# Performance work log

Measured on AMD Instinct MI355X. Metric: run time of the kernel, lower is better.

## Reference

```python
import jax, jax.numpy as jnp
import numpy as np

H = 512        # rnn_h
E = 256        # embedding_dim
ATD = 32       # action_type_emb_dim
VOCAB = 50000  # data_agent.wordcnt
NUM_ACTIONS = 10
CHECK_WEIGHT = 1.0
B, SIN, SOUT, Y = 32, 128, 32, 256
DIN = 2 * H + 1 + E + ATD + E  # dec_gru input size (y_in=True, bidir=True)


def gru_step(h, x, Wih, Whh, bih, bhh):
    # PyTorch GRUCell math
    gi = x @ Wih.T + bih
    gh = h @ Whh.T + bhh
    ir, iz, i_n = jnp.split(gi, 3, axis=-1)
    hr, hz, h_n = jnp.split(gh, 3, axis=-1)
    r = jax.nn.sigmoid(ir + hr)
    z = jax.nn.sigmoid(iz + hz)
    n = jnp.tanh(i_n + r * h_n)
    return (1.0 - z) * n + z * h


def setup_inputs() -> dict:
    key = jax.random.key(0)
    ks = iter(jax.random.split(key, 48))

    def p(shape, scale=0.05):
        return jax.random.normal(next(ks), shape, dtype=jnp.float32) * scale

    inp = {}
    inp["x"] = jax.random.randint(next(ks), (B, SIN), 0, VOCAB)
    inp["action_key"] = jax.random.randint(next(ks), (Y,), 0, VOCAB)
    inp["action_type"] = jax.random.randint(next(ks), (Y,), 0, NUM_ACTIONS + 1)
    inp["current_room"] = jax.random.randint(next(ks), (B, SOUT), 0, VOCAB)
    inp["checked"] = jax.random.uniform(next(ks), (B, SOUT + 1, Y), dtype=jnp.float32)
    inp["y"] = jax.random.uniform(next(ks), (B, SOUT, Y), dtype=jnp.float32)
    emb = p((VOCAB, E))
    inp["emb_table"] = emb.at[0].set(0.0)  # padding_idx=0
    inp["atype_table"] = p((NUM_ACTIONS + 1, ATD))
    # encoder GRU, bidirectional, 1 layer
    inp["enc_Wih_f"] = p((3 * H, E)); inp["enc_Whh_f"] = p((3 * H, H))
    inp["enc_bih_f"] = p((3 * H,));   inp["enc_bhh_f"] = p((3 * H,))
    inp["enc_Wih_b"] = p((3 * H, E)); inp["enc_Whh_b"] = p((3 * H, H))
    inp["enc_bih_b"] = p((3 * H,));   inp["enc_bhh_b"] = p((3 * H,))
    inp["trans_W"] = p((E, 2 * H)); inp["trans_b"] = p((E,))
    inp["merge_W"] = p((H, 2 * H)); inp["merge_b"] = p((H,))
    inp["dec_Wih"] = p((3 * H, DIN)); inp["dec_Whh"] = p((3 * H, H))
    inp["dec_bih"] = p((3 * H,));     inp["dec_bhh"] = p((3 * H,))
    inp["dec_W"] = p((1, H)); inp["dec_b"] = p((1,))
    inp["chk_W1"] = p((H, 2 * H + ATD + H)); inp["chk_b1"] = p((H,))
    inp["chk_W2"] = p((1, H));               inp["chk_b2"] = p((1,))
    return inp


def reference(x, action_key, action_type, current_room, checked, y,
              emb_table, atype_table,
              enc_Wih_f, enc_Whh_f, enc_bih_f, enc_bhh_f,
              enc_Wih_b, enc_Whh_b, enc_bih_b, enc_bhh_b,
              trans_W, trans_b, merge_W, merge_b,
              dec_Wih, dec_Whh, dec_bih, dec_bhh, dec_W, dec_b,
              chk_W1, chk_b1, chk_W2, chk_b2):
    emb_out = emb_table[x]  # [B, SIN, E]

    def enc_scan(Wih, Whh, bih, bhh, xs):  # xs: [S, B, E]
        def step(h, xt):
            h2 = gru_step(h, xt, Wih, Whh, bih, bhh)
            return h2, h2
        h0 = jnp.zeros((B, H), emb_out.dtype)
        return jax.lax.scan(step, h0, xs)

    xs = emb_out.transpose(1, 0, 2)
    hT_f, hs_f = enc_scan(enc_Wih_f, enc_Whh_f, enc_bih_f, enc_bhh_f, xs)
    hT_b, hs_b = enc_scan(enc_Wih_b, enc_Whh_b, enc_bih_b, enc_bhh_b, xs[::-1])
    hs_b = hs_b[::-1]
    enc_out = jnp.concatenate([hs_f, hs_b], axis=-1).transpose(1, 0, 2)  # [B, SIN, 2H]

    action_emb = emb_table[action_key]  # [Y, E]
    trans_out = jnp.tanh(enc_out @ trans_W.T + trans_b)  # [B, SIN, E]
    scores = (jnp.einsum('bse,ye->bys', emb_out, action_emb)
              + jnp.einsum('bse,ye->bys', trans_out, action_emb))
    alpha = jax.nn.softmax(scores, axis=-1)
    attention = jnp.einsum('bys,bsd->byd', alpha, enc_out)  # [B, Y, 2H]

    atype_exp = jnp.broadcast_to(atype_table[action_type], (B, Y, ATD))
    room_emb = emb_table[current_room]  # [B, SOUT, E]

    # faithful to torch: hidden [2,B,H].view(B, 2H) (layer-major flatten)
    hidden_cat = jnp.stack([hT_f, hT_b], 0).reshape(B, 2 * H)
    h0_dec = jnp.tanh(hidden_cat @ merge_W.T + merge_b)  # [B, H]
    h_dec = jnp.broadcast_to(h0_dec[:, None, :], (B, Y, H)).reshape(B * Y, H)

    y_prev = jnp.concatenate([jnp.zeros((B, 1, Y), y.dtype), y[:, :-1]], axis=1)

    att_flat = attention.reshape(B * Y, 2 * H)
    at_flat = atype_exp.reshape(B * Y, ATD)

    xs_scan = (checked[:, :SOUT].transpose(1, 0, 2),   # check_in  [T,B,Y]
               room_emb.transpose(1, 0, 2),            # room      [T,B,E]
               y_prev.transpose(1, 0, 2),              # y_{t-1}   [T,B,Y]
               y.transpose(1, 0, 2),                   # y_t       [T,B,Y]
               checked[:, 1:].transpose(1, 0, 2))      # check tgt [T,B,Y]

    def step(h, inputs):
        chk_t, room_t, yp_t, y_t, chk_next = inputs
        room_in = jnp.broadcast_to(room_t[:, None, :], (B, Y, E))
        y_in = jnp.broadcast_to((yp_t @ action_emb)[:, None, :], (B, Y, E))
        dec_in = jnp.concatenate(
            [attention, chk_t[..., None], room_in, atype_exp, y_in], axis=-1
        ).reshape(B * Y, DIN)
        h2 = gru_step(h, dec_in, dec_Wih, dec_Whh, dec_bih, dec_bhh)
        logits = (h2 @ dec_W.T + dec_b).reshape(B, Y)
        logp = jax.nn.log_softmax(logits, axis=1)
        l = -(logp * y_t).sum()
        cat = jnp.concatenate([att_flat, at_flat, h2], axis=1)
        chk = jax.nn.sigmoid(jnp.tanh(cat @ chk_W1.T + chk_b1) @ chk_W2.T + chk_b2).reshape(B, Y)
        cl = -((chk_next * jnp.log(chk) + (1.0 - chk_next) * jnp.log(1.0 - chk)) * y_t).sum() * CHECK_WEIGHT
        return h2, (l, cl)

    _, (ls, cls) = jax.lax.scan(step, h_dec, xs_scan)
    ysum = y.sum()
    loss = ls.sum() / ysum
    check_loss = cls.sum() / ysum
    return (loss + check_loss, loss, check_loss)
```

## Files before the change

kernel.cpp:

```cpp
#include <hip/hip_runtime.h>

typedef unsigned short ushort;
typedef unsigned int uint;
typedef __attribute__((ext_vector_type(8))) short short8;
typedef __attribute__((ext_vector_type(4))) float f32x4;
typedef __attribute__((ext_vector_type(4))) uint u32x4;

#define DEVI __device__ __forceinline__

#define B_ 32
#define SIN_ 128
#define SOUT_ 32
#define Y_ 256
#define H_ 512
#define E_ 256
#define TH_ 1536

DEVI float b2f(ushort u){ return __uint_as_float(((uint)u)<<16); }
DEVI ushort f2b(float f){ uint x = __float_as_uint(f); return (ushort)((x + 0x7FFFu + ((x>>16)&1u)) >> 16); }
DEVI float sigf(float x){ return 1.f/(1.f+__expf(-x)); }
DEVI float tanh_fast(float x){ return 2.f/(1.f+__expf(-2.f*x)) - 1.f; }
DEVI float splus(float x){ return fmaxf(x,0.f) + log1pf(__expf(-fabsf(x))); }
DEVI short8 cvt8(u32x4 v){ return __builtin_bit_cast(short8, v); }

DEVI uint ld_flag(const uint* p){
  uint r;
  asm volatile("global_load_dword %0, %1, off sc0 sc1\n\ts_waitcnt vmcnt(0)"
               : "=v"(r) : "v"(p) : "memory");
  return r;
}
DEVI void st_flag(uint* p, uint v){
  asm volatile("global_store_dword %0, %1, off sc0 sc1" :: "v"(p), "v"(v) : "memory");
}
DEVI void st_h16(ushort* p, uint v){
  asm volatile("global_store_short %0, %1, off sc0 sc1" :: "v"(p), "v"(v) : "memory");
}

__global__ void k_init(float* acc){ if (threadIdx.x < 4) acc[threadIdx.x] = 0.f; }

__global__ void k_wsfail(float* out){ out[0]=1.2345e8f; out[1]=2.3456e8f; out[2]=3.4567e8f; }

__global__ void k_init_enc(uint* __restrict__ flags, ushort* __restrict__ hG)
{
  const int id = blockIdx.x*256 + threadIdx.x;
  if (id < 256) flags[id] = 0u;
  if (id < 16384) ((uint4*)hG)[id] = make_uint4(0,0,0,0);
}

__global__ __launch_bounds__(256) void k_ysum(const float* __restrict__ yv, float* __restrict__ acc)
{
  __shared__ float red[256];
  float s = 0.f;
  for (long i = (long)blockIdx.x*256 + threadIdx.x; i < (long)B_*SOUT_*Y_; i += (long)gridDim.x*256) s += yv[i];
  red[threadIdx.x] = s; __syncthreads();
  for (int o=128;o;o>>=1){ if ((int)threadIdx.x<o) red[threadIdx.x] += red[threadIdx.x+o]; __syncthreads(); }
  if (threadIdx.x==0) atomicAdd(acc+2, red[0]);
}

__global__ void k_lookup(const int* __restrict__ x, const int* __restrict__ akey,
                         const int* __restrict__ atype, const int* __restrict__ croom,
                         const float* __restrict__ yv,
                         const float* __restrict__ emb, const float* __restrict__ attab,
                         ushort* __restrict__ embxs, ushort* __restrict__ aemb,
                         ushort* __restrict__ aembT, float* __restrict__ avec,
                         ushort* __restrict__ acat, ushort* __restrict__ yprev)
{
  const long N1 = (long)SIN_*B_*E_;
  const long N2 = (long)Y_*E_;
  const long N3 = (long)Y_*32;
  const long N4 = (long)SOUT_*B_*E_;
  const long N5 = (long)SOUT_*B_*Y_;
  for (long i = (long)blockIdx.x*blockDim.x + threadIdx.x; i < N1+N2+N3+N4+N5; i += (long)gridDim.x*blockDim.x){
    long id = i;
    if (id < N1){
      int e = id & 255; long sb = id >> 8; int bb = (int)(sb & 31); int s = (int)(sb >> 5);
      embxs[id] = f2b(emb[(size_t)x[bb*SIN_ + s]*E_ + e]);
    } else if ((id -= N1) < N2){
      int e = (int)(id & 255), yy = (int)(id >> 8);
      ushort v = f2b(emb[(size_t)akey[yy]*E_ + e]);
      aemb[yy*E_ + e] = v;
      aembT[e*Y_ + yy] = v;
    } else if ((id -= N2) < N3){
      int a = (int)(id & 31), yy = (int)(id >> 5);
      avec[yy*32 + a] = attab[atype[yy]*32 + a];
    } else if ((id -= N3) < N4){
      int e = (int)(id & 255); long tb = id >> 8; int bb = (int)(tb & 31); int t = (int)(tb >> 5);
      acat[(size_t)tb*512 + e] = f2b(emb[(size_t)croom[bb*SOUT_ + t]*E_ + e]);
    } else { id -= N4;
      int yy = (int)(id & 255); long tb = id >> 8; int bb = (int)(tb & 31); int t = (int)(tb >> 5);
      yprev[id] = (t == 0) ? (ushort)0 : f2b(yv[((size_t)bb*SOUT_ + (t-1))*Y_ + yy]);
    }
  }
}

__global__ __launch_bounds__(256)
void k_convall(const float* __restrict__ eWihF, const float* __restrict__ eWihB,
               const float* __restrict__ transW, const float* __restrict__ dWih,
               const float* __restrict__ cW1, const float* __restrict__ dWhh,
               ushort* __restrict__ WihFb, ushort* __restrict__ WihBb,
// ... 219 lines not shown
  const int brow0 = mi*16 + l4*4;

  const float* W = dir ? Wb : Wf;
  const float* bh = dir ? bhb : bhf;
  const ushort* gi = dir ? gib : gif;

  __shared__ __align__(16) float cred[2][3][256];
  __shared__ float bhl[48];

  short8 bw[3][8];
  {
    const int kbase = kh*256 + l4*8;
    #pragma unroll
    for (int ni=0; ni<3; ++ni){
      const float* wr = W + (size_t)(ni*512 + j0 + l15)*512 + kbase;
      #pragma unroll
      for (int ks=0; ks<8; ++ks){
        const float4 f0 = *(const float4*)(wr + ks*32);
        const float4 f1 = *(const float4*)(wr + ks*32 + 4);
        short8 v;
        v[0]=(short)f2b(f0.x); v[1]=(short)f2b(f0.y); v[2]=(short)f2b(f0.z); v[3]=(short)f2b(f0.w);
        v[4]=(short)f2b(f1.x); v[5]=(short)f2b(f1.y); v[6]=(short)f2b(f1.z); v[7]=(short)f2b(f1.w);
        bw[ni][ks] = v;
      }
    }
  }
  if (tid < 48) bhl[tid] = bh[(tid>>4)*512 + j0 + (tid&15)];
  __syncthreads();

  float bh0r=0.f, bh1r=0.f, bh2r=0.f;
  if (kh==0){ bh0r = bhl[l15]; bh1r = bhl[16+l15]; bh2r = bhl[32+l15]; }
  float holdr[4] = {0.f,0.f,0.f,0.f};
  uint* myflag = flags + dir*32 + (g&31);

  for (int t=0; t<128; ++t){
    const int tt = dir ? (127 - t) : t;
    float giv0[4], giv1[4], giv2[4];
    if (kh==0){
      const ushort* girow = gi + ((size_t)tt*32 + brow0)*1536 + j0 + l15;
      #pragma unroll
      for (int q=0; q<4; ++q){
        giv0[q] = b2f(girow[q*1536]);
        giv1[q] = b2f(girow[q*1536 + 512]);
        giv2[q] = b2f(girow[q*1536 + 1024]);
      }
    }
    if (t){
      if ((tid>>6)==2 && (tid&63)<32){
        const uint* fp = flags + dir*32 + (tid&31);
        while (ld_flag(fp) < (uint)t) __builtin_amdgcn_s_sleep(2);
      }
      __syncthreads();
    }
    const ushort* hsrc = hG + ((size_t)((t&1)*2 + dir))*32768 + (size_t)(mi*16+l15)*1024 + kh*256 + l4*8;
    u32x4 a0,a1,a2,a3,a4,a5,a6,a7,b0,b1,b2,b3,b4,b5,b6,b7;
    asm volatile(
      "global_load_dwordx4 %0, %16, off sc0 sc1\n\t"
      "global_load_dwordx4 %1, %16, off offset:64 sc0 sc1\n\t"
      "global_load_dwordx4 %2, %16, off offset:128 sc0 sc1\n\t"
      "global_load_dwordx4 %3, %16, off offset:192 sc0 sc1\n\t"
      "global_load_dwordx4 %4, %16, off offset:256 sc0 sc1\n\t"
      "global_load_dwordx4 %5, %16, off offset:320 sc0 sc1\n\t"
      "global_load_dwordx4 %6, %16, off offset:384 sc0 sc1\n\t"
      "global_load_dwordx4 %7, %16, off offset:448 sc0 sc1\n\t"
      "global_load_dwordx4 %8, %16, off offset:1024 sc0 sc1\n\t"
      "global_load_dwordx4 %9, %16, off offset:1088 sc0 sc1\n\t"
      "global_load_dwordx4 %10, %16, off offset:1152 sc0 sc1\n\t"
      "global_load_dwordx4 %11, %16, off offset:1216 sc0 sc1\n\t"
      "global_load_dwordx4 %12, %16, off offset:1280 sc0 sc1\n\t"
      "global_load_dwordx4 %13, %16, off offset:1344 sc0 sc1\n\t"
      "global_load_dwordx4 %14, %16, off offset:1408 sc0 sc1\n\t"
      "global_load_dwordx4 %15, %16, off offset:1472 sc0 sc1\n\t"
      "s_waitcnt vmcnt(0)"
      : "=&v"(a0),"=&v"(a1),"=&v"(a2),"=&v"(a3),"=&v"(a4),"=&v"(a5),"=&v"(a6),"=&v"(a7),
        "=&v"(b0),"=&v"(b1),"=&v"(b2),"=&v"(b3),"=&v"(b4),"=&v"(b5),"=&v"(b6),"=&v"(b7)
      : "v"(hsrc)
      : "memory");
    const short8 ah[8] = {cvt8(a0),cvt8(a1),cvt8(a2),cvt8(a3),cvt8(a4),cvt8(a5),cvt8(a6),cvt8(a7)};
    const short8 al[8] = {cvt8(b0),cvt8(b1),cvt8(b2),cvt8(b3),cvt8(b4),cvt8(b5),cvt8(b6),cvt8(b7)};
    f32x4 acc[3]; acc[0]=0.f; acc[1]=0.f; acc[2]=0.f;
    #pragma unroll
    for (int ks=0; ks<8; ++ks){
      acc[0] = __builtin_amdgcn_mfma_f32_16x16x32_bf16(ah[ks], bw[0][ks], acc[0],0,0,0);
      acc[1] = __builtin_amdgcn_mfma_f32_16x16x32_bf16(ah[ks], bw[1][ks], acc[1],0,0,0);
      acc[2] = __builtin_amdgcn_mfma_f32_16x16x32_bf16(ah[ks], bw[2][ks], acc[2],0,0,0);
      acc[0] = __builtin_amdgcn_mfma_f32_16x16x32_bf16(al[ks], bw[0][ks], acc[0],0,0,0);
      acc[1] = __builtin_amdgcn_mfma_f32_16x16x32_bf16(al[ks], bw[1][ks], acc[1],0,0,0);
      acc[2] = __builtin_amdgcn_mfma_f32_16x16x32_bf16(al[ks], bw[2][ks], acc[2],0,0,0);
    }
    if (kh==1){
      #pragma unroll
      for (int ni=0; ni<3; ++ni) *(f32x4*)&cred[mi][ni][lane*4] = acc[ni];
    }
    __syncthreads();
    if (kh==0){
      #pragma unroll
      for (int ni=0; ni<3; ++ni){
        const f32x4 o = *(const f32x4*)&cred[mi][ni][lane*4];
        acc[ni][0]+=o[0]; acc[ni][1]+=o[1]; acc[ni][2]+=o[2]; acc[ni][3]+=o[3];
      }
      ushort* dst = hG + ((size_t)(((t+1)&1)*2 + dir))*32768;
      #pragma unroll
      for (int q=0; q<4; ++q){
        const int b = brow0 + q;
        const float r  = sigf(giv0[q] + acc[0][q] + bh0r);
        const float zg = sigf(giv1[q] + acc[1][q] + bh1r);
        const float n  = tanh_fast(giv2[q] + r*(acc[2][q] + bh2r));
        const float h2 = (1.f - zg)*n + zg*holdr[q];
        holdr[q] = h2;
        const ushort hb = f2b(h2);
        const ushort hl = f2b(h2 - b2f(hb));
        if (t < 127){
          st_h16(dst + (size_t)b*1024 + j0 + l15, (uint)hb);
          st_h16(dst + (size_t)b*1024 + 512 + j0 + l15, (uint)hl);
        }
        encout[((size_t)b*SIN_ + tt)*1024 + dir*H_ + j0 + l15] = hb;
        encoutT[((size_t)b*1024 + dir*H_ + j0 + l15)*SIN_ + tt] = hb;
      }
    }
    __syncthreads();
    if (t < 127 && tid == 0) st_flag(myflag, (uint)(t+1));
  }
  if (kh==0){
    float* hT = dir ? hTb : hTf;
    #pragma unroll
    for (int q=0; q<4; ++q) hT[(size_t)(brow0+q)*H_ + j0 + l15] = holdr[q];
  }
}

__global__ __launch_bounds__(256) void k_softmax(const float* __restrict__ sc, ushort* __restrict__ al)
{
  const int row = blockIdx.x*4 + (threadIdx.x>>6);
  const int lane = threadIdx.x&63;
  const float* s = sc + (size_t)row*SIN_;
  const float2 v = *(const float2*)&s[lane*2];
  float m = fmaxf(v.x, v.y);
  #pragma unroll
  for (int o=1;o<64;o<<=1) m = fmaxf(m, __shfl_xor(m, o));
  const float e0 = __expf(v.x - m), e1 = __expf(v.y - m);
  float sum = e0 + e1;
  #pragma unroll
  for (int o=1;o<64;o<<=1) sum += __shfl_xor(sum, o);
  const float inv = 1.f/sum;
  ushort* a = al + (size_t)row*SIN_;
  const uint pkv = (uint)f2b(e0*inv) | ((uint)f2b(e1*inv)<<16);
  *(uint*)&a[lane*2] = pkv;
}

__global__ __launch_bounds__(512)
void k_merge(const float* __restrict__ hTf, const float* __restrict__ hTb,
             const float* __restrict__ mW, const float* __restrict__ mb,
             float* __restrict__ h0)
{
  const int b = blockIdx.x, j = threadIdx.x;
  __shared__ float hc[1024];
  for (int i=j; i<1024; i+=512){
    const int half = i >> 9, jj = i & 511;
    hc[i] = (b < 16) ? hTf[(size_t)(2*b + half)*H_ + jj] : hTb[(size_t)(2*(b-16) + half)*H_ + jj];
  }
  __syncthreads();
  float d = mb[j];
  const float* wr = mW + (size_t)j*1024;
  #pragma unroll 8
  for (int k=0;k<1024;k+=4){
    const float4 a = *(const float4*)&wr[k];
    const float4 hh = *(const float4*)&hc[k];
    d += a.x*hh.x + a.y*hh.y + a.z*hh.z + a.w*hh.w;
  }
  h0[(size_t)b*H_ + j] = tanh_fast(d);
}

__global__ void k_bcast(const float* __restrict__ h0, ushort* __restrict__ hb,
                        float* __restrict__ chkdot, float* __restrict__ logits)
{
  for (long i = (long)blockIdx.x*blockDim.x + threadIdx.x; i < (long)8192*H_; i += (long)gridDim.x*blockDim.x){
    const int jj = (int)(i & 511); const long row = i >> 9; const int bb = (int)(row >> 8);
    hb[i] = f2b(h0[(size_t)bb*H_ + jj]);
    if (i < 8192){ chkdot[i] = 0.f; logits[i] = 0.f; }
  }
}

__global__ __launch_bounds__(512,1)
void gemm_dec(const ushort* __restrict__ A, const ushort* __restrict__ Wd,
              const ushort* __restrict__ gib, const float* __restrict__ sproj_t,
              const float* __restrict__ wchk, const float* __restrict__ dbhh,
              const float* __restrict__ checked, int t,
              const float* __restrict__ decW,
              ushort* __restrict__ h2bo, float* __restrict__ logits)
{
  const int bx = blockIdx.x;
  const int by = blockIdx.y;
  const int bm = by<<7;
  const int tid = threadIdx.x;
  const int w = tid>>6, lane = tid&63;
  const int wrh = w>>2, wc = w&3;
  const int wm = wrh<<6;
  const int l15 = lane&15, l4 = lane>>4;
  __shared__ ushort lsA[128*72];
  __shared__ ushort lsB[384*72];
  f32x4 acc[3][4][2];
  #pragma unroll
  for (int gg=0;gg<3;++gg)
    #pragma unroll
    for (int mi2=0;mi2<4;++mi2)
      #pragma unroll
      for (int ni2=0;ni2<2;++ni2) acc[gg][mi2][ni2] = 0.f;

  const int saRow0 = tid>>3, saK = (tid&7)<<3;
  uint4 va[2], vb[6];
  {
    #pragma unroll
    for (int i=0;i<2;++i){
      const int row = saRow0 + (i<<6);
      va[i] = *(const uint4*)&A[(size_t)(bm+row)*512 + saK];
    }
    #pragma unroll
    for (int i=0;i<6;++i){
      const int s = tid + (i<<9);
      const int gg = s>>10, w1 = s&1023, row = w1>>3, kc = (w1&7)<<3;
      vb[i] = *(const uint4*)&Wd[(size_t)((gg<<9) + (bx<<7) + row)*512 + kc];
    }
  }
  for (int kt=0; kt<8; ++kt){
    __syncthreads();
    #pragma unroll
    for (int i=0;i<2;++i){
      const int row = saRow0 + (i<<6);
      *(uint4*)&lsA[row*72 + saK] = va[i];
    }
    #pragma unroll
    for (int i=0;i<6;++i){
      const int s = tid + (i<<9);
      const int gg = s>>10, w1 = s&1023, row = w1>>3, kc = (w1&7)<<3;
      *(uint4*)&lsB[((gg<<7)+row)*72 + kc] = vb[i];
    }
    __syncthreads();
    if (kt < 7){
      const int ko = (kt+1)<<6;
      #pragma unroll
      for (int i=0;i<2;++i){
        const int row = saRow0 + (i<<6);
        va[i] = *(const uint4*)&A[(size_t)(bm+row)*512 + ko + saK];
      }
      #pragma unroll
      for (int i=0;i<6;++i){
        const int s = tid + (i<<9);
        const int gg = s>>10, w1 = s&1023, row = w1>>3, kc = (w1&7)<<3;
        vb[i] = *(const uint4*)&Wd[(size_t)((gg<<9) + (bx<<7) + row)*512 + ko + kc];
      }
    }
    #pragma unroll
    for (int ks=0;ks<2;++ks){
      short8 af[4];
      #pragma unroll
      for (int mi2=0;mi2<4;++mi2)
        af[mi2] = *(const short8*)&lsA[(wm + (mi2<<4) + l15)*72 + (ks<<5) + (l4<<3)];
      short8 bf[3][2];
      #pragma unroll
      for (int gg=0;gg<3;++gg)
        #pragma unroll
        for (int ni2=0;ni2<2;++ni2)
          bf[gg][ni2] = *(const short8*)&lsB[((gg<<7) + (wc<<5) + (ni2<<4) + l15)*72 + (ks<<5) + (l4<<3)];
      #pragma unroll
      for (int gg=0;gg<3;++gg)
        #pragma unroll
        for (int mi2=0;mi2<4;++mi2)
          #pragma unroll
          for (int ni2=0;ni2<2;++ni2)
            acc[gg][mi2][ni2] = __builtin_amdgcn_mfma_f32_16x16x32_bf16(af[mi2], bf[gg][ni2], acc[gg][mi2][ni2], 0,0,0);
    }
  }
  const int bb = by>>1;
  const float* sp = sproj_t + (size_t)bb*TH_;
  const int jbase = (bx<<7) + (wc<<5);
  float spv[3][2], wcv[3][2], bhnv[2], dwv[2];
  #pragma unroll
  for (int ni2=0;ni2<2;++ni2){
    const int j = jbase + (ni2<<4) + l15;
    spv[0][ni2] = sp[j]; spv[1][ni2] = sp[512+j]; spv[2][ni2] = sp[1024+j];
    wcv[0][ni2] = wchk[j]; wcv[1][ni2] = wchk[512+j]; wcv[2][ni2] = wchk[1024+j];
    bhnv[ni2] = dbhh[1024+j];
    dwv[ni2] = decW[j];
  }
  const float* ckrow = checked + ((size_t)(bb*33 + t))*Y_;
  float lrow[4][4];
  #pragma unroll
  for (int mi2=0;mi2<4;++mi2)
    #pragma unroll
    for (int q=0;q<4;++q) lrow[mi2][q] = 0.f;
  #pragma unroll
  for (int mi2=0;mi2<4;++mi2){
    #pragma unroll
    for (int q=0;q<4;++q){
      const int row = bm + wm + (mi2<<4) + (l4<<2) + q;
      const float ck = ckrow[row & 255];
      #pragma unroll
      for (int ni2=0;ni2<2;++ni2){
        const int j = jbase + (ni2<<4) + l15;
        const float g0 = b2f(gib[(size_t)row*TH_ + j]);
        const float g1 = b2f(gib[(size_t)row*TH_ + 512 + j]);
        const float g2 = b2f(gib[(size_t)row*TH_ + 1024 + j]);
        const float hold = b2f(A[(size_t)row*H_ + j]);
        const float r  = sigf(g0 + spv[0][ni2] + ck*wcv[0][ni2] + acc[0][mi2][ni2][q]);
        const float zg = sigf(g1 + spv[1][ni2] + ck*wcv[1][ni2] + acc[1][mi2][ni2][q]);
        const float n  = tanh_fast(g2 + spv[2][ni2] + ck*wcv[2][ni2] + r*(acc[2][mi2][ni2][q] + bhnv[ni2]));
        const float h2 = (1.f - zg)*n + zg*hold;
        h2bo[(size_t)row*H_ + j] = f2b(h2);
        lrow[mi2][q] += h2 * dwv[ni2];
      }
    }
  }
  #pragma unroll
  for (int mi2=0;mi2<4;++mi2)
    #pragma unroll
    for (int q=0;q<4;++q){
      float v = lrow[mi2][q];
      v += __shfl_xor(v,1); v += __shfl_xor(v,2); v += __shfl_xor(v,4); v += __shfl_xor(v,8);
      if (l15==0){
        const int row = bm + wm + (mi2<<4) + (l4<<2) + q;
        atomicAdd(&logits[row], v);
      }
    }
}

__global__ __launch_bounds__(256)
void dec_loss(float* __restrict__ chkdot, const float* __restrict__ cb2v,
              const float* __restrict__ checked, const float* __restrict__ yv,
              float* __restrict__ logits, int t, float* __restrict__ acc)
{
  const int tid = threadIdx.x;
  if (blockIdx.x < 32){
    const int row = blockIdx.x*256 + tid;
    const int bb = row>>8, yy = row&255;
    const float u = chkdot[row] + cb2v[0];
    chkdot[row] = 0.f;
    const float c = checked[((size_t)bb*33 + (t+1))*Y_ + yy];
    const float yt = yv[((size_t)bb*SOUT_ + t)*Y_ + yy];
    float wv = yt * (c*splus(-u) + (1.f-c)*splus(u));
    __shared__ float red[256];
    red[tid] = wv; __syncthreads();
    for (int o=128;o;o>>=1){ if (tid<o) red[tid] += red[tid+o]; __syncthreads(); }
    if (tid==0) atomicAdd(acc+1, red[0]);
  } else {
    __shared__ float red[256];
    __shared__ float bmx[32], bsm[32];
    const int bb = tid>>3, part = tid&7;
    float lv[32];
    const float* lg = logits + bb*Y_ + part*32;
    float m = -1e30f;
    #pragma unroll
    for (int i=0;i<32;++i){ lv[i] = lg[i]; m = fmaxf(m, lv[i]); }
    red[tid] = m; __syncthreads();
    if (part==0){ float mm = red[tid];
      #pragma unroll
      for (int k2=1;k2<8;++k2) mm = fmaxf(mm, red[tid+k2]);
      bmx[bb] = mm; }
    __syncthreads();
    const float bm = bmx[bb];
    float se = 0.f;
    #pragma unroll
    for (int i=0;i<32;++i) se += __expf(lv[i]-bm);
    red[tid] = se; __syncthreads();
    if (part==0){ float ss = 0.f;
      #pragma unroll
      for (int k2=0;k2<8;++k2) ss += red[tid+k2];
      bsm[bb] = ss; }
    __syncthreads();
    const float lse = bm + logf(bsm[bb]);
    const float* yr = yv + ((size_t)bb*SOUT_ + t)*Y_ + part*32;
    float pl = 0.f;
    #pragma unroll
    for (int i=0;i<32;++i) pl += yr[i]*(lv[i]-lse);
    red[tid] = pl; __syncthreads();
    if (tid==0){ float s = 0.f;
      for (int k2=0;k2<256;++k2) s += red[k2];
      atomicAdd(acc+0, -s); }
    __syncthreads();
    for (int i=tid; i<8192; i+=256) logits[i] = 0.f;
  }
}

__global__ void k_final(const float* __restrict__ acc, float* __restrict__ out)
{
  if (threadIdx.x==0){
    const float ls = acc[0], cls = acc[1], ys = acc[2];
    out[0] = (ls+cls)/ys; out[1] = ls/ys; out[2] = cls/ys;
  }
}

extern "C" void kernel_launch(void* const* d_in, const int* in_sizes, int n_in,
                              void* d_out, int out_size, void* d_ws, size_t ws_size,
                              hipStream_t stream)
{
  (void)in_sizes; (void)n_in; (void)out_size;
  const int*   x      = (const int*)d_in[0];
  const int*   akey   = (const int*)d_in[1];
  const int*   atype  = (const int*)d_in[2];
  const int*   croom  = (const int*)d_in[3];
  const float* checked= (const float*)d_in[4];
  const float* yv     = (const float*)d_in[5];
  const float* emb    = (const float*)d_in[6];
  const float* attab  = (const float*)d_in[7];
  const float* eWihF  = (const float*)d_in[8];
  const float* eWhhF  = (const float*)d_in[9];
  const float* ebihF  = (const float*)d_in[10];
  const float* ebhhF  = (const float*)d_in[11];
  const float* eWihB  = (const float*)d_in[12];
  const float* eWhhB  = (const float*)d_in[13];
  const float* ebihB  = (const float*)d_in[14];
  const float* ebhhB  = (const float*)d_in[15];
  const float* transW = (const float*)d_in[16];
  const float* transb = (const float*)d_in[17];
  const float* mergeW = (const float*)d_in[18];
  const float* mergeb = (const float*)d_in[19];
  const float* dWih   = (const float*)d_in[20];
  const float* dWhh   = (const float*)d_in[21];
  const float* dbih   = (const float*)d_in[22];
  const float* dbhh   = (const float*)d_in[23];
  const float* dW     = (const float*)d_in[24];
  const float* cW1    = (const float*)d_in[26];
  const float* cb1    = (const float*)d_in[27];
  const float* cW2    = (const float*)d_in[28];
  const float* cb2    = (const float*)d_in[29];

  char* base = (char*)d_ws;
  size_t off = 0;
  auto alloc = [&](size_t bytes)->char*{ char* p = base + off; off += (bytes + 255) & ~(size_t)255; return p; };

  float*  accv   = (float*)alloc(256);
  ushort* embxs  = (ushort*)alloc((size_t)SIN_*B_*E_*2);
  ushort* aemb   = (ushort*)alloc((size_t)Y_*E_*2);
  ushort* aembT  = (ushort*)alloc((size_t)Y_*E_*2);
  float*  avec   = (float*)alloc((size_t)Y_*32*4);
  ushort* yprev  = (ushort*)alloc((size_t)SOUT_*B_*Y_*2);
  ushort* acat   = (ushort*)alloc((size_t)SOUT_*B_*512*2);
  ushort* gi_fb  = (ushort*)alloc((size_t)2*SIN_*B_*TH_*2);
  ushort* gi_f   = gi_fb;
  ushort* gi_b   = gi_fb + (size_t)SIN_*B_*TH_;
  ushort* gibase = gi_fb;
  ushort* encout = (ushort*)alloc((size_t)B_*SIN_*1024*2);
  ushort* encoutT= (ushort*)alloc((size_t)B_*1024*SIN_*2);
  float*  hTf    = (float*)alloc((size_t)B_*H_*4);
  float*  hTb    = (float*)alloc((size_t)B_*H_*4);
  float*  h0dec  = (float*)alloc((size_t)B_*H_*4);
  ushort* esum   = (ushort*)alloc((size_t)B_*SIN_*E_*2);
  float*  scores = (float*)alloc((size_t)B_*Y_*SIN_*4);
  ushort* alpha  = (ushort*)alloc((size_t)B_*Y_*SIN_*2);
  ushort* att    = (ushort*)alloc((size_t)8192*1024*2);
  ushort* chkbase= (ushort*)alloc((size_t)8192*H_*2);
  float*  addy   = (float*)alloc((size_t)Y_*TH_*4);
  float*  addcy  = (float*)alloc((size_t)Y_*H_*4);
  float*  sproj  = (float*)alloc((size_t)SOUT_*B_*TH_*4);
  float*  wchk   = (float*)alloc((size_t)TH_*4);
  float*  dbhhrz = (float*)alloc((size_t)TH_*4);
  ushort* WihFb  = (ushort*)alloc((size_t)TH_*E_*2);
  ushort* WihBb  = (ushort*)alloc((size_t)TH_*E_*2);
  ushort* Wtrb   = (ushort*)alloc((size_t)E_*1024*2);
  ushort* Wattb  = (ushort*)alloc((size_t)TH_*1024*2);
  ushort* Wcat2b = (ushort*)alloc((size_t)TH_*512*2);
  ushort* W1attb = (ushort*)alloc((size_t)H_*1024*2);
  ushort* Wdecb  = (ushort*)alloc((size_t)TH_*512*2);
  ushort* Wchk2b = (ushort*)alloc((size_t)512*512*2);
  ushort* h2bA   = (ushort*)alloc((size_t)8192*H_*2);
  ushort* h2bB   = (ushort*)alloc((size_t)8192*H_*2);
  float*  chkdot = (float*)alloc((size_t)8192*4);
  float*  logits = (float*)alloc((size_t)8192*4);
  ushort* hG     = (ushort*)alloc((size_t)2*2*32*1024*2);
  uint*   flags  = (uint*)alloc((size_t)256*4);

  if (off > ws_size){ k_wsfail<<<1,1,0,stream>>>((float*)d_out); return; }

  float* outp = (float*)d_out;

  k_init<<<dim3(1), dim3(64), 0, stream>>>(accv);
  k_init_enc<<<dim3(64), dim3(256), 0, stream>>>(flags, hG);
  k_ysum<<<dim3(256), dim3(256), 0, stream>>>(yv, accv);
  k_lookup<<<dim3(2048), dim3(256), 0, stream>>>(x, akey, atype, croom, yv, emb, attab,
                                                 embxs, aemb, aembT, avec, acat, yprev);
  k_convall<<<dim3(2048), dim3(256), 0, stream>>>(eWihF, eWihB, transW, dWih, cW1, dWhh,
                                                  WihFb, WihBb, Wtrb, Wattb, Wcat2b, W1attb, Wdecb, Wchk2b);
  k_prep2<<<dim3(1024), dim3(256), 0, stream>>>(avec, dWih, dbih, cW1, cb1, dbhh,
                                                addy, addcy, wchk, dbhhrz);

  gemm_nt<(GF_BIAS|GF_WBF16)><<<dim3(12,32,1), dim3(256), 0, stream>>>(
    embxs, WihFb, ebihF, nullptr, 0, nullptr, gi_f, TH_, E_, E_, E_, 0, 0L,0L,0L, nullptr);
  gemm_nt<(GF_BIAS|GF_WBF16)><<<dim3(12,32,1), dim3(256), 0, stream>>>(
    embxs, WihBb, ebihB, nullptr, 0, nullptr, gi_b, TH_, E_, E_, E_, 0, 0L,0L,0L, nullptr);

  enc_persist<<<dim3(64), dim3(256), 0, stream>>>(eWhhF, eWhhB, ebhhF, ebhhB, gi_f, gi_b,
                                                  hG, flags, encout, encoutT, hTf, hTb);

  gemm_nt<(GF_BIAS|GF_TANH|GF_ESUM|GF_WBF16)><<<dim3(2,32,1), dim3(256), 0, stream>>>(
    encout, Wtrb, transb, nullptr, 0, nullptr, esum, E_, 1024, 1024, 1024, 0, 0L,0L,0L, embxs);

  gemm_nt<GF_WF32><<<dim3(1,2,32), dim3(256), 0, stream>>>(
    aemb, esum, nullptr, nullptr, 0, scores, nullptr, SIN_, E_, E_, E_, 0,
    0L, (long)SIN_*E_, (long)Y_*SIN_, nullptr);
  k_softmax<<<dim3(2048), dim3(256), 0, stream>>>(scores, alpha);

  gemm_nt<GF_WBF16><<<dim3(8,2,32), dim3(256), 0, stream>>>(
    alpha, encoutT, nullptr, nullptr, 0, nullptr, att, 1024, SIN_, SIN_, SIN_, 0,
    (long)Y_*SIN_, (long)1024*SIN_, (long)Y_*1024, nullptr);

  k_merge<<<dim3(32), dim3(512), 0, stream>>>(hTf, hTb, mergeW, mergeb, h0dec);

  gemm_nt<GF_WBF16><<<dim3(2,8,1), dim3(256), 0, stream>>>(
    yprev, aembT, nullptr, nullptr, 0, nullptr, acat+256, 512, Y_, Y_, Y_, 0, 0L,0L,0L, nullptr);
  gemm_nt<(GF_BIAS|GF_WF32)><<<dim3(12,8,1), dim3(256), 0, stream>>>(
    acat, Wcat2b, dbhhrz, nullptr, 0, sproj, nullptr, TH_, 512, 512, 512, 0, 0L,0L,0L, nullptr);

  gemm_nt<(GF_WBF16|GF_ADDY)><<<dim3(12,64,1), dim3(256), 0, stream>>>(
    att, Wattb, nullptr, addy, TH_, nullptr, gibase, TH_, 1024, 1024, 1024, 0, 0L,0L,0L, nullptr);
  gemm_nt<(GF_WBF16|GF_ADDY)><<<dim3(4,64,1), dim3(256), 0, stream>>>(
    att, W1attb, nullptr, addcy, H_, nullptr, chkbase, H_, 1024, 1024, 1024, 0, 0L,0L,0L, nullptr);

  k_bcast<<<dim3(4096), dim3(256), 0, stream>>>(h0dec, h2bA, chkdot, logits);

  for (int t=0; t<SOUT_; ++t){
    ushort* hin_b  = (t&1) ? h2bB : h2bA;
    ushort* hout_b = (t&1) ? h2bA : h2bB;
    gemm_dec<<<dim3(4,64), dim3(512), 0, stream>>>(
      hin_b, Wdecb, gibase, sproj + (size_t)t*B_*TH_, wchk, dbhh, checked, t,
      dW, hout_b, logits);
    gemm_nt<GF_CHK><<<dim3(4,64), dim3(256), 0, stream>>>(
      hout_b, Wchk2b, nullptr, cW2, 0, chkdot, nullptr, 0, 512, 512, 512, 0,
      0L,0L,0L, chkbase);
    dec_loss<<<dim3(33), dim3(256), 0, stream>>>(chkdot, cb2, checked, yv, logits, t, accv);
  }
  k_final<<<dim3(1), dim3(1), 0, stream>>>(accv, outp);
}
```

Before: 4.077 ms.

## Fuse decoder loss into next-step GRU kernel and drop encoder hi/lo split

The per-step dec_loss launch is folded into the decoder GRU kernel as extra blocks that compute the previous step's check and softmax losses. Logit and check buffers are double-buffered so the loss work overlaps the next GRU step, and the launch count per step drops from three to two. Separately, the encoder recurrent state exchange now stores only a bf16 hidden state instead of hi+lo bf16 pairs, halving the loads and MFMAs on the serial encoder path at some precision cost. The encoder output stores are also moved after the flag release so they are off the cross-block critical path.

```diff
diff --git a/kernel.cpp b/kernel.cpp
--- a/kernel.cpp
+++ b/kernel.cpp
@@ -44,7 +44,7 @@
 {
   const int id = blockIdx.x*256 + threadIdx.x;
   if (id < 256) flags[id] = 0u;
-  if (id < 16384) ((uint4*)hG)[id] = make_uint4(0,0,0,0);
+  if (id < 8192) ((uint4*)hG)[id] = make_uint4(0,0,0,0);
 }
 
 __global__ __launch_bounds__(256) void k_ysum(const float* __restrict__ yv, float* __restrict__ acc)
@@ -370,54 +370,42 @@
       }
       __syncthreads();
     }
-    const ushort* hsrc = hG + ((size_t)((t&1)*2 + dir))*32768 + (size_t)(mi*16+l15)*1024 + kh*256 + l4*8;
-    u32x4 a0,a1,a2,a3,a4,a5,a6,a7,b0,b1,b2,b3,b4,b5,b6,b7;
+    const ushort* hsrc = hG + ((size_t)((t&1)*2 + dir))*16384 + (size_t)(mi*16+l15)*512 + kh*256 + l4*8;
+    u32x4 a0,a1,a2,a3,a4,a5,a6,a7;
     asm volatile(
-      "global_load_dwordx4 %0, %16, off sc0 sc1\n\t"
-      "global_load_dwordx4 %1, %16, off offset:64 sc0 sc1\n\t"
-      "global_load_dwordx4 %2, %16, off offset:128 sc0 sc1\n\t"
-      "global_load_dwordx4 %3, %16, off offset:192 sc0 sc1\n\t"
-      "global_load_dwordx4 %4, %16, off offset:256 sc0 sc1\n\t"
-      "global_load_dwordx4 %5, %16, off offset:320 sc0 sc1\n\t"
-      "global_load_dwordx4 %6, %16, off offset:384 sc0 sc1\n\t"
-      "global_load_dwordx4 %7, %16, off offset:448 sc0 sc1\n\t"
-      "global_load_dwordx4 %8, %16, off offset:1024 sc0 sc1\n\t"
-      "global_load_dwordx4 %9, %16, off offset:1088 sc0 sc1\n\t"
-      "global_load_dwordx4 %10, %16, off offset:1152 sc0 sc1\n\t"
-      "global_load_dwordx4 %11, %16, off offset:1216 sc0 sc1\n\t"
-      "global_load_dwordx4 %12, %16, off offset:1280 sc0 sc1\n\t"
-      "global_load_dwordx4 %13, %16, off offset:1344 sc0 sc1\n\t"
-      "global_load_dwordx4 %14, %16, off offset:1408 sc0 sc1\n\t"
-      "global_load_dwordx4 %15, %16, off offset:1472 sc0 sc1\n\t"
+      "global_load_dwordx4 %0, %8, off sc0 sc1\n\t"
+      "global_load_dwordx4 %1, %8, off offset:64 sc0 sc1\n\t"
+      "global_load_dwordx4 %2, %8, off offset:128 sc0 sc1\n\t"
+      "global_load_dwordx4 %3, %8, off offset:192 sc0 sc1\n\t"
+      "global_load_dwordx4 %4, %8, off offset:256 sc0 sc1\n\t"
+      "global_load_dwordx4 %5, %8, off offset:320 sc0 sc1\n\t"
+      "global_load_dwordx4 %6, %8, off offset:384 sc0 sc1\n\t"
+      "global_load_dwordx4 %7, %8, off offset:448 sc0 sc1\n\t"
       "s_waitcnt vmcnt(0)"
-      : "=&v"(a0),"=&v"(a1),"=&v"(a2),"=&v"(a3),"=&v"(a4),"=&v"(a5),"=&v"(a6),"=&v"(a7),
-        "=&v"(b0),"=&v"(b1),"=&v"(b2),"=&v"(b3),"=&v"(b4),"=&v"(b5),"=&v"(b6),"=&v"(b7)
+      : "=&v"(a0),"=&v"(a1),"=&v"(a2),"=&v"(a3),"=&v"(a4),"=&v"(a5),"=&v"(a6),"=&v"(a7)
       : "v"(hsrc)
       : "memory");
     const short8 ah[8] = {cvt8(a0),cvt8(a1),cvt8(a2),cvt8(a3),cvt8(a4),cvt8(a5),cvt8(a6),cvt8(a7)};
-    const short8 al[8] = {cvt8(b0),cvt8(b1),cvt8(b2),cvt8(b3),cvt8(b4),cvt8(b5),cvt8(b6),cvt8(b7)};
     f32x4 acc[3]; acc[0]=0.f; acc[1]=0.f; acc[2]=0.f;
     #pragma unroll
     for (int ks=0; ks<8; ++ks){
       acc[0] = __builtin_amdgcn_mfma_f32_16x16x32_bf16(ah[ks], bw[0][ks], acc[0],0,0,0);
       acc[1] = __builtin_amdgcn_mfma_f32_16x16x32_bf16(ah[ks], bw[1][ks], acc[1],0,0,0);
       acc[2] = __builtin_amdgcn_mfma_f32_16x16x32_bf16(ah[ks], bw[2][ks], acc[2],0,0,0);
-      acc[0] = __builtin_amdgcn_mfma_f32_16x16x32_bf16(al[ks], bw[0][ks], acc[0],0,0,0);
-      acc[1] = __builtin_amdgcn_mfma_f32_16x16x32_bf16(al[ks], bw[1][ks], acc[1],0,0,0);
-      acc[2] = __builtin_amdgcn_mfma_f32_16x16x32_bf16(al[ks], bw[2][ks], acc[2],0,0,0);
     }
     if (kh==1){
       #pragma unroll
       for (int ni=0; ni<3; ++ni) *(f32x4*)&cred[mi][ni][lane*4] = acc[ni];
     }
     __syncthreads();
+    ushort hbs[4];
     if (kh==0){
       #pragma unroll
       for (int ni=0; ni<3; ++ni){
         const f32x4 o = *(const f32x4*)&cred[mi][ni][lane*4];
         acc[ni][0]+=o[0]; acc[ni][1]+=o[1]; acc[ni][2]+=o[2]; acc[ni][3]+=o[3];
       }
-      ushort* dst = hG + ((size_t)(((t+1)&1)*2 + dir))*32768;
+      ushort* dst = hG + ((size_t)(((t+1)&1)*2 + dir))*16384;
       #pragma unroll
       for (int q=0; q<4; ++q){
         const int b = brow0 + q;
@@ -427,17 +415,20 @@
         const float h2 = (1.f - zg)*n + zg*holdr[q];
         holdr[q] = h2;
         const ushort hb = f2b(h2);
-        const ushort hl = f2b(h2 - b2f(hb));
-        if (t < 127){
-          st_h16(dst + (size_t)b*1024 + j0 + l15, (uint)hb);
-          st_h16(dst + (size_t)b*1024 + 512 + j0 + l15, (uint)hl);
-        }
-        encout[((size_t)b*SIN_ + tt)*1024 + dir*H_ + j0 + l15] = hb;
-        encoutT[((size_t)b*1024 + dir*H_ + j0 + l15)*SIN_ + tt] = hb;
+        hbs[q] = hb;
+        if (t < 127) st_h16(dst + (size_t)b*512 + j0 + l15, (uint)hb);
       }
     }
     __syncthreads();
     if (t < 127 && tid == 0) st_flag(myflag, (uint)(t+1));
+    if (kh==0){
+      #pragma unroll
+      for (int q=0; q<4; ++q){
+        const int b = brow0 + q;
+        encout[((size_t)b*SIN_ + tt)*1024 + dir*H_ + j0 + l15] = hbs[q];
+        encoutT[((size_t)b*1024 + dir*H_ + j0 + l15)*SIN_ + tt] = hbs[q];
+      }
+    }
   }
   if (kh==0){
     float* hT = dir ? hTb : hTf;
@@ -489,212 +480,206 @@
 }
 
 __global__ void k_bcast(const float* __restrict__ h0, ushort* __restrict__ hb,
-                        float* __restrict__ chkdot, float* __restrict__ logits)
+                        float* __restrict__ L0, float* __restrict__ L1,
+                        float* __restrict__ C0, float* __restrict__ C1)
 {
   for (long i = (long)blockIdx.x*blockDim.x + threadIdx.x; i < (long)8192*H_; i += (long)gridDim.x*blockDim.x){
     const int jj = (int)(i & 511); const long row = i >> 9; const int bb = (int)(row >> 8);
     hb[i] = f2b(h0[(size_t)bb*H_ + jj]);
-    if (i < 8192){ chkdot[i] = 0.f; logits[i] = 0.f; }
+    if (i < 8192){ L0[i] = 0.f; L1[i] = 0.f; C0[i] = 0.f; C1[i] = 0.f; }
   }
 }
 
 __global__ __launch_bounds__(512,1)
-void gemm_dec(const ushort* __restrict__ A, const ushort* __restrict__ Wd,
-              const ushort* __restrict__ gib, const float* __restrict__ sproj_t,
-              const float* __restrict__ wchk, const float* __restrict__ dbhh,
-              const float* __restrict__ checked, int t,
-              const float* __restrict__ decW,
-              ushort* __restrict__ h2bo, float* __restrict__ logits)
-{
-  const int bx = blockIdx.x;
-  const int by = blockIdx.y;
-  const int bm = by<<7;
+void gemm_dec2(const ushort* __restrict__ A, const ushort* __restrict__ Wd,
+               const ushort* __restrict__ gib, const float* __restrict__ sproj_t,
+               const float* __restrict__ wchk, const float* __restrict__ dbhh,
+               const float* __restrict__ checked, int t,
+               const float* __restrict__ decW,
+               ushort* __restrict__ h2bo, float* __restrict__ LW,
+               float* __restrict__ chkdotR, const float* __restrict__ cb2v,
+               const float* __restrict__ yv, float* __restrict__ LR,
+               float* __restrict__ accv)
+{
+  __shared__ __align__(16) ushort smem[36864];
   const int tid = threadIdx.x;
-  const int w = tid>>6, lane = tid&63;
-  const int wrh = w>>2, wc = w&3;
-  const int wm = wrh<<6;
-  const int l15 = lane&15, l4 = lane>>4;
-  __shared__ ushort lsA[128*72];
-  __shared__ ushort lsB[384*72];
-  f32x4 acc[3][4][2];
-  #pragma unroll
-  for (int gg=0;gg<3;++gg)
-    #pragma unroll
-    for (int mi2=0;mi2<4;++mi2)
-      #pragma unroll
-      for (int ni2=0;ni2<2;++ni2) acc[gg][mi2][ni2] = 0.f;
-
-  const int saRow0 = tid>>3, saK = (tid&7)<<3;
-  uint4 va[2], vb[6];
-  {
-    #pragma unroll
-    for (int i=0;i<2;++i){
-      const int row = saRow0 + (i<<6);
-      va[i] = *(const uint4*)&A[(size_t)(bm+row)*512 + saK];
-    }
-    #pragma unroll
-    for (int i=0;i<6;++i){
-      const int s = tid + (i<<9);
-      const int gg = s>>10, w1 = s&1023, row = w1>>3, kc = (w1&7)<<3;
-      vb[i] = *(const uint4*)&Wd[(size_t)((gg<<9) + (bx<<7) + row)*512 + kc];
-    }
-  }
-  for (int kt=0; kt<8; ++kt){
-    __syncthreads();
-    #pragma unroll
-    for (int i=0;i<2;++i){
-      const int row = saRow0 + (i<<6);
-      *(uint4*)&lsA[row*72 + saK] = va[i];
-    }
-    #pragma unroll
-    for (int i=0;i<6;++i){
-      const int s = tid + (i<<9);
-      const int gg = s>>10, w1 = s&1023, row = w1>>3, kc = (w1&7)<<3;
-      *(uint4*)&lsB[((gg<<7)+row)*72 + kc] = vb[i];
-    }
-    __syncthreads();
-    if (kt < 7){
-      const int ko = (kt+1)<<6;
+
+  if (blockIdx.x < 256){
+    if (t >= SOUT_) return;
+    const int bx = blockIdx.x & 3;
+    const int by = blockIdx.x >> 2;
+    const int bm = by<<7;
+    const int w = tid>>6, lane = tid&63;
+    const int wrh = w>>2, wc = w&3;
+    const int wm = wrh<<6;
+    const int l15 = lane&15, l4 = lane>>4;
+    ushort* lsA = smem;
+    ushort* lsB = smem + 128*72;
+    f32x4 acc[3][4][2];
+    #pragma unroll
+    for (int gg=0;gg<3;++gg)
+      #pragma unroll
+      for (int mi2=0;mi2<4;++mi2)
+        #pragma unroll
+        for (int ni2=0;ni2<2;++ni2) acc[gg][mi2][ni2] = 0.f;
+
+    const int saRow0 = tid>>3, saK = (tid&7)<<3;
+    uint4 va[2], vb[6];
+    {
       #pragma unroll
       for (int i=0;i<2;++i){
         const int row = saRow0 + (i<<6);
-        va[i] = *(const uint4*)&A[(size_t)(bm+row)*512 + ko + saK];
+        va[i] = *(const uint4*)&A[(size_t)(bm+row)*512 + saK];
       }
       #pragma unroll
       for (int i=0;i<6;++i){
         const int s = tid + (i<<9);
         const int gg = s>>10, w1 = s&1023, row = w1>>3, kc = (w1&7)<<3;
-        vb[i] = *(const uint4*)&Wd[(size_t)((gg<<9) + (bx<<7) + row)*512 + ko + kc];
-      }
-    }
-    #pragma unroll
-    for (int ks=0;ks<2;++ks){
-      short8 af[4];
-      #pragma unroll
-      for (int mi2=0;mi2<4;++mi2)
-        af[mi2] = *(const short8*)&lsA[(wm + (mi2<<4) + l15)*72 + (ks<<5) + (l4<<3)];
-      short8 bf[3][2];
-      #pragma unroll
-      for (int gg=0;gg<3;++gg)
-        #pragma unroll
-        for (int ni2=0;ni2<2;++ni2)
-          bf[gg][ni2] = *(const short8*)&lsB[((gg<<7) + (wc<<5) + (ni2<<4) + l15)*72 + (ks<<5) + (l4<<3)];
-      #pragma unroll
-      for (int gg=0;gg<3;++gg)
+        vb[i] = *(const uint4*)&Wd[(size_t)((gg<<9) + (bx<<7) + row)*512 + kc];
+      }
+    }
+    for (int kt=0; kt<8; ++kt){
+      __syncthreads();
+      #pragma unroll
+      for (int i=0;i<2;++i){
+        const int row = saRow0 + (i<<6);
+        *(uint4*)&lsA[row*72 + saK] = va[i];
+      }
+      #pragma unroll
+      for (int i=0;i<6;++i){
+        const int s = tid + (i<<9);
+        const int gg = s>>10, w1 = s&1023, row = w1>>3, kc = (w1&7)<<3;
+        *(uint4*)&lsB[((gg<<7)+row)*72 + kc] = vb[i];
+      }
+      __syncthreads();
+      if (kt < 7){
+        const int ko = (kt+1)<<6;
+        #pragma unroll
+        for (int i=0;i<2;++i){
+          const int row = saRow0 + (i<<6);
+          va[i] = *(const uint4*)&A[(size_t)(bm+row)*512 + ko + saK];
+        }
+        #pragma unroll
+        for (int i=0;i<6;++i){
+          const int s = tid + (i<<9);
+          const int gg = s>>10, w1 = s&1023, row = w1>>3, kc = (w1&7)<<3;
+          vb[i] = *(const uint4*)&Wd[(size_t)((gg<<9) + (bx<<7) + row)*512 + ko + kc];
+        }
+      }
+      #pragma unroll
+      for (int ks=0;ks<2;++ks){
+        short8 af[4];
         #pragma unroll
         for (int mi2=0;mi2<4;++mi2)
+          af[mi2] = *(const short8*)&lsA[(wm + (mi2<<4) + l15)*72 + (ks<<5) + (l4<<3)];
+        short8 bf[3][2];
+        #pragma unroll
+        for (int gg=0;gg<3;++gg)
           #pragma unroll
           for (int ni2=0;ni2<2;++ni2)
-            acc[gg][mi2][ni2] = __builtin_amdgcn_mfma_f32_16x16x32_bf16(af[mi2], bf[gg][ni2], acc[gg][mi2][ni2], 0,0,0);
-    }
-  }
-  const int bb = by>>1;
-  const float* sp = sproj_t + (size_t)bb*TH_;
-  const int jbase = (bx<<7) + (wc<<5);
-  float spv[3][2], wcv[3][2], bhnv[2], dwv[2];
-  #pragma unroll
-  for (int ni2=0;ni2<2;++ni2){
-    const int j = jbase + (ni2<<4) + l15;
-    spv[0][ni2] = sp[j]; spv[1][ni2] = sp[512+j]; spv[2][ni2] = sp[1024+j];
-    wcv[0][ni2] = wchk[j]; wcv[1][ni2] = wchk[512+j]; wcv[2][ni2] = wchk[1024+j];
-    bhnv[ni2] = dbhh[1024+j];
-    dwv[ni2] = decW[j];
-  }
-  const float* ckrow = checked + ((size_t)(bb*33 + t))*Y_;
-  float lrow[4][4];
-  #pragma unroll
-  for (int mi2=0;mi2<4;++mi2)
-    #pragma unroll
-    for (int q=0;q<4;++q) lrow[mi2][q] = 0.f;
-  #pragma unroll
-  for (int mi2=0;mi2<4;++mi2){
-    #pragma unroll
-    for (int q=0;q<4;++q){
-      const int row = bm + wm + (mi2<<4) + (l4<<2) + q;
-      const float ck = ckrow[row & 255];
-      #pragma unroll
-      for (int ni2=0;ni2<2;++ni2){
-        const int j = jbase + (ni2<<4) + l15;
-        const float g0 = b2f(gib[(size_t)row*TH_ + j]);
-        const float g1 = b2f(gib[(size_t)row*TH_ + 512 + j]);
-        const float g2 = b2f(gib[(size_t)row*TH_ + 1024 + j]);
-        const float hold = b2f(A[(size_t)row*H_ + j]);
-        const float r  = sigf(g0 + spv[0][ni2] + ck*wcv[0][ni2] + acc[0][mi2][ni2][q]);
-        const float zg = sigf(g1 + spv[1][ni2] + ck*wcv[1][ni2] + acc[1][mi2][ni2][q]);
-        const float n  = tanh_fast(g2 + spv[2][ni2] + ck*wcv[2][ni2] + r*(acc[2][mi2][ni2][q] + bhnv[ni2]));
-        const float h2 = (1.f - zg)*n + zg*hold;
-        h2bo[(size_t)row*H_ + j] = f2b(h2);
-        lrow[mi2][q] += h2 * dwv[ni2];
-      }
-    }
-  }
-  #pragma unroll
-  for (int mi2=0;mi2<4;++mi2)
-    #pragma unroll
-    for (int q=0;q<4;++q){
-      float v = lrow[mi2][q];
-      v += __shfl_xor(v,1); v += __shfl_xor(v,2); v += __shfl_xor(v,4); v += __shfl_xor(v,8);
-      if (l15==0){
+            bf[gg][ni2] = *(const short8*)&lsB[((gg<<7) + (wc<<5) + (ni2<<4) + l15)*72 + (ks<<5) + (l4<<3)];
+        #pragma unroll
+        for (int gg=0;gg<3;++gg)
+          #pragma unroll
+          for (int mi2=0;mi2<4;++mi2)
+            #pragma unroll
+            for (int ni2=0;ni2<2;++ni2)
+              acc[gg][mi2][ni2] = __builtin_amdgcn_mfma_f32_16x16x32_bf16(af[mi2], bf[gg][ni2], acc[gg][mi2][ni2], 0,0,0);
+      }
+    }
+    const int bb = by>>1;
+    const float* sp = sproj_t + (size_t)bb*TH_;
+    const int jbase = (bx<<7) + (wc<<5);
+    float spv[3][2], wcv[3][2], bhnv[2], dwv[2];
+    #pragma unroll
+    for (int ni2=0;ni2<2;++ni2){
+      const int j = jbase + (ni2<<4) + l15;
+      spv[0][ni2] = sp[j]; spv[1][ni2] = sp[512+j]; spv[2][ni2] = sp[1024+j];
+      wcv[0][ni2] = wchk[j]; wcv[1][ni2] = wchk[512+j]; wcv[2][ni2] = wchk[1024+j];
+      bhnv[ni2] = dbhh[1024+j];
+      dwv[ni2] = decW[j];
+    }
+    const float* ckrow = checked + ((size_t)(bb*33 + t))*Y_;
+    float lrow[4][4];
+    #pragma unroll
+    for (int mi2=0;mi2<4;++mi2)
+      #pragma unroll
+      for (int q=0;q<4;++q) lrow[mi2][q] = 0.f;
+    #pragma unroll
+    for (int mi2=0;mi2<4;++mi2){
+      #pragma unroll
+      for (int q=0;q<4;++q){
         const int row = bm + wm + (mi2<<4) + (l4<<2) + q;
-        atomicAdd(&logits[row], v);
-      }
-    }
-}
-
-__global__ __launch_bounds__(256)
-void dec_loss(float* __restrict__ chkdot, const float* __restrict__ cb2v,
-              const float* __restrict__ checked, const float* __restrict__ yv,
-              float* __restrict__ logits, int t, float* __restrict__ acc)
-{
-  const int tid = threadIdx.x;
-  if (blockIdx.x < 32){
-    const int row = blockIdx.x*256 + tid;
-    const int bb = row>>8, yy = row&255;
-    const float u = chkdot[row] + cb2v[0];
-    chkdot[row] = 0.f;
-    const float c = checked[((size_t)bb*33 + (t+1))*Y_ + yy];
-    const float yt = yv[((size_t)bb*SOUT_ + t)*Y_ + yy];
-    float wv = yt * (c*splus(-u) + (1.f-c)*splus(u));
-    __shared__ float red[256];
-    red[tid] = wv; __syncthreads();
-    for (int o=128;o;o>>=1){ if (tid<o) red[tid] += red[tid+o]; __syncthreads(); }
-    if (tid==0) atomicAdd(acc+1, red[0]);
+        const float ck = ckrow[row & 255];
+        #pragma unroll
+        for (int ni2=0;ni2<2;++ni2){
+          const int j = jbase + (ni2<<4) + l15;
+          const float g0 = b2f(gib[(size_t)row*TH_ + j]);
+          const float g1 = b2f(gib[(size_t)row*TH_ + 512 + j]);
+          const float g2 = b2f(gib[(size_t)row*TH_ + 1024 + j]);
+          const float hold = b2f(A[(size_t)row*H_ + j]);
+          const float r  = sigf(g0 + spv[0][ni2] + ck*wcv[0][ni2] + acc[0][mi2][ni2][q]);
+          const float zg = sigf(g1 + spv[1][ni2] + ck*wcv[1][ni2] + acc[1][mi2][ni2][q]);
+          const float n  = tanh_fast(g2 + spv[2][ni2] + ck*wcv[2][ni2] + r*(acc[2][mi2][ni2][q] + bhnv[ni2]));
+          const float h2 = (1.f - zg)*n + zg*hold;
+          h2bo[(size_t)row*H_ + j] = f2b(h2);
+          lrow[mi2][q] += h2 * dwv[ni2];
+        }
+      }
+    }
+    #pragma unroll
+    for (int mi2=0;mi2<4;++mi2)
+      #pragma unroll
+      for (int q=0;q<4;++q){
+        float v = lrow[mi2][q];
+        v += __shfl_xor(v,1); v += __shfl_xor(v,2); v += __shfl_xor(v,4); v += __shfl_xor(v,8);
+        if (l15==0){
+          const int row = bm + wm + (mi2<<4) + (l4<<2) + q;
+          atomicAdd(&LW[row], v);
+        }
+      }
   } else {
-    __shared__ float red[256];
-    __shared__ float bmx[32], bsm[32];
-    const int bb = tid>>3, part = tid&7;
-    float lv[32];
-    const float* lg = logits + bb*Y_ + part*32;
-    float m = -1e30f;
-    #pragma unroll
-    for (int i=0;i<32;++i){ lv[i] = lg[i]; m = fmaxf(m, lv[i]); }
-    red[tid] = m; __syncthreads();
-    if (part==0){ float mm = red[tid];
-      #pragma unroll
-      for (int k2=1;k2<8;++k2) mm = fmaxf(mm, red[tid+k2]);
-      bmx[bb] = mm; }
-    __syncthreads();
-    const float bm = bmx[bb];
-    float se = 0.f;
-    #pragma unroll
-    for (int i=0;i<32;++i) se += __expf(lv[i]-bm);
-    red[tid] = se; __syncthreads();
-    if (part==0){ float ss = 0.f;
-      #pragma unroll
-      for (int k2=0;k2<8;++k2) ss += red[tid+k2];
-      bsm[bb] = ss; }
-    __syncthreads();
-    const float lse = bm + logf(bsm[bb]);
-    const float* yr = yv + ((size_t)bb*SOUT_ + t)*Y_ + part*32;
-    float pl = 0.f;
-    #pragma unroll
-    for (int i=0;i<32;++i) pl += yr[i]*(lv[i]-lse);
-    red[tid] = pl; __syncthreads();
-    if (tid==0){ float s = 0.f;
-      for (int k2=0;k2<256;++k2) s += red[k2];
-      atomicAdd(acc+0, -s); }
-    __syncthreads();
-    for (int i=tid; i<8192; i+=256) logits[i] = 0.f;
+    if (t == 0) return;
+    const int km1 = t - 1;
+    const int lb = blockIdx.x - 256;
+    float* red = (float*)smem;
+    if (lb < 16){
+      const int row = lb*512 + tid;
+      const int bb = row>>8, yy = row&255;
+      const float u = chkdotR[row] + cb2v[0];
+      chkdotR[row] = 0.f;
+      const float c = checked[((size_t)bb*33 + km1 + 1)*Y_ + yy];
+      const float yt = yv[((size_t)bb*SOUT_ + km1)*Y_ + yy];
+      red[tid] = yt * (c*splus(-u) + (1.f-c)*splus(u));
+      __syncthreads();
+      for (int o=256;o;o>>=1){ if (tid<o) red[tid] += red[tid+o]; __syncthreads(); }
+      if (tid==0) atomicAdd(accv+1, red[0]);
+    } else {
+      const int bb = tid>>4, part = tid&15;
+      const float* lg = LR + bb*Y_ + part*16;
+      float lv[16];
+      float m = -1e30f;
+      #pragma unroll
+      for (int i=0;i<16;++i){ lv[i] = lg[i]; m = fmaxf(m, lv[i]); }
+      m = fmaxf(m, __shfl_xor(m,1)); m = fmaxf(m, __shfl_xor(m,2));
+      m = fmaxf(m, __shfl_xor(m,4)); m = fmaxf(m, __shfl_xor(m,8));
+      float se = 0.f;
+      #pragma unroll
+      for (int i=0;i<16;++i) se += __expf(lv[i]-m);
+      se += __shfl_xor(se,1); se += __shfl_xor(se,2); se += __shfl_xor(se,4); se += __shfl_xor(se,8);
+      const float lse = m + logf(se);
+      const float* yr = yv + ((size_t)bb*SOUT_ + km1)*Y_ + part*16;
+      float pl = 0.f;
+      #pragma unroll
+      for (int i=0;i<16;++i) pl += yr[i]*(lv[i]-lse);
+      pl += __shfl_xor(pl,1); pl += __shfl_xor(pl,2); pl += __shfl_xor(pl,4); pl += __shfl_xor(pl,8);
+      red[tid] = (part==0) ? pl : 0.f;
+      __syncthreads();
+      for (int o=256;o;o>>=1){ if (tid<o) red[tid] += red[tid+o]; __syncthreads(); }
+      if (tid==0) atomicAdd(accv+0, -red[0]);
+      __syncthreads();
+      for (int i=tid; i<8192; i+=512) LR[i] = 0.f;
+    }
   }
 }
 
@@ -781,9 +766,11 @@
   ushort* Wchk2b = (ushort*)alloc((size_t)512*512*2);
   ushort* h2bA   = (ushort*)alloc((size_t)8192*H_*2);
   ushort* h2bB   = (ushort*)alloc((size_t)8192*H_*2);
-  float*  chkdot = (float*)alloc((size_t)8192*4);
-  float*  logits = (float*)alloc((size_t)8192*4);
-  ushort* hG     = (ushort*)alloc((size_t)2*2*32*1024*2);
+  float*  C0     = (float*)alloc((size_t)8192*4);
+  float*  C1     = (float*)alloc((size_t)8192*4);
+  float*  L0     = (float*)alloc((size_t)8192*4);
+  float*  L1     = (float*)alloc((size_t)8192*4);
+  ushort* hG     = (ushort*)alloc((size_t)2*2*32*512*2);
   uint*   flags  = (uint*)alloc((size_t)256*4);
 
   if (off > ws_size){ k_wsfail<<<1,1,0,stream>>>((float*)d_out); return; }
@@ -832,18 +819,24 @@
   gemm_nt<(GF_WBF16|GF_ADDY)><<<dim3(4,64,1), dim3(256), 0, stream>>>(
     att, W1attb, nullptr, addcy, H_, nullptr, chkbase, H_, 1024, 1024, 1024, 0, 0L,0L,0L, nullptr);
 
-  k_bcast<<<dim3(4096), dim3(256), 0, stream>>>(h0dec, h2bA, chkdot, logits);
-
-  for (int t=0; t<SOUT_; ++t){
-    ushort* hin_b  = (t&1) ? h2bB : h2bA;
-    ushort* hout_b = (t&1) ? h2bA : h2bB;
-    gemm_dec<<<dim3(4,64), dim3(512), 0, stream>>>(
-      hin_b, Wdecb, gibase, sproj + (size_t)t*B_*TH_, wchk, dbhh, checked, t,
-      dW, hout_b, logits);
-    gemm_nt<GF_CHK><<<dim3(4,64), dim3(256), 0, stream>>>(
-      hout_b, Wchk2b, nullptr, cW2, 0, chkdot, nullptr, 0, 512, 512, 512, 0,
-      0L,0L,0L, chkbase);
-    dec_loss<<<dim3(33), dim3(256), 0, stream>>>(chkdot, cb2, checked, yv, logits, t, accv);
+  k_bcast<<<dim3(1024), dim3(256), 0, stream>>>(h0dec, h2bA, L0, L1, C0, C1);
+
+  for (int k=0; k<=SOUT_; ++k){
+    const ushort* hin = (k&1) ? h2bB : h2bA;
+    ushort* hout      = (k&1) ? h2bA : h2bB;
+    float* LWp = (k&1) ? L1 : L0;
+    float* LRp = (k&1) ? L0 : L1;
+    float* Cw  = (k&1) ? C1 : C0;
+    float* Cr  = (k&1) ? C0 : C1;
+    const int ks = (k < SOUT_) ? k : 0;
+    gemm_dec2<<<dim3(273), dim3(512), 0, stream>>>(
+      hin, Wdecb, gibase, sproj + (size_t)ks*B_*TH_, wchk, dbhh, checked, k,
+      dW, hout, LWp, Cr, cb2, yv, LRp, accv);
+    if (k < SOUT_){
+      gemm_nt<GF_CHK><<<dim3(4,64), dim3(256), 0, stream>>>(
+        hout, Wchk2b, nullptr, cW2, 0, Cw, nullptr, 0, 512, 512, 512, 0,
+        0L,0L,0L, chkbase);
+    }
   }
   k_final<<<dim3(1), dim3(1), 0, stream>>>(accv, outp);
 }
```

Result: faster. 3.935 ms (-3.5%).
